# Performance work log

Hardware: AMD Instinct MI355X
Metric: run time of the kernel (lower is better)

## Reference

```python
import jax, jax.numpy as jnp
import numpy as np

B, N, C = 2, 2048, 1024
H = 16
D = C // H  # 64
EPS = 1e-6


def rms_norm(x, w):
    # LlamaRMSNorm: fp32 variance over last dim
    xf = x.astype(jnp.float32)
    var = jnp.mean(xf * xf, axis=-1, keepdims=True)
    xf = xf * jax.lax.rsqrt(var + EPS)
    return (w * xf).astype(x.dtype)


def setup_inputs() -> dict:
    key = jax.random.key(0)
    ks = jax.random.split(key, 4)
    x = jax.random.normal(ks[0], (B, N, C), dtype=jnp.float32)
    mask = jax.random.randint(ks[1], (B, N), 0, 2, dtype=jnp.int32)
    qkv_w = jax.random.normal(ks[2], (3 * C, C), dtype=jnp.float32) * (1.0 / np.sqrt(C))
    qkv_b = jnp.zeros((3 * C,), dtype=jnp.float32)
    proj_w = jax.random.normal(ks[3], (C, C), dtype=jnp.float32) * (1.0 / np.sqrt(C))
    proj_b = jnp.zeros((C,), dtype=jnp.float32)
    qn_w = jnp.ones((D,), dtype=jnp.float32)
    kn_w = jnp.ones((D,), dtype=jnp.float32)
    return {"x": x, "mask": mask, "qkv_w": qkv_w, "qkv_b": qkv_b,
            "proj_w": proj_w, "proj_b": proj_b, "qn_w": qn_w, "kn_w": kn_w}


def reference(x, mask, qkv_w, qkv_b, proj_w, proj_b, qn_w, kn_w):
    dtype = x.dtype
    scale = D ** -0.5
    # qkv projection -> (3, B, H, N, D)
    qkv = (x @ qkv_w.T + qkv_b).reshape(B, N, 3, H, D).transpose(2, 0, 3, 1, 4)
    q, k, v = qkv[0], qkv[1], qkv[2]
    q = rms_norm(q, qn_w)
    k = rms_norm(k, kn_w)
    q = q * scale
    # scores in fp32, key-padding mask [B,1,1,N]
    attn = jnp.einsum('bhnd,bhmd->bhnm', q, k).astype(jnp.float32)
    key_mask = (mask != 0)[:, None, None, :]
    attn = jnp.where(key_mask, attn, jnp.float32(-1e9))
    attn = jax.nn.softmax(attn, axis=-1).astype(dtype)
    out = jnp.einsum('bhnm,bhmd->bhnd', attn, v)  # (B,H,N,D)
    out = out.transpose(0, 2, 1, 3).reshape(B, N, C)
    return out @ proj_w.T + proj_b
```

## Files before the change

### kernel.cpp

```cpp
#include <hip/hip_runtime.h>
#include <hip/hip_bf16.h>
#include <stdint.h>

namespace {

constexpr int kB = 2;
constexpr int kN = 2048;
constexpr int kC = 1024;
constexpr int kH = 16;
constexpr int kD = 64;
constexpr int kTok = kB * kN;
constexpr int k3C  = 3 * kC;
constexpr size_t kPS = (size_t)kTok * k3C;
constexpr size_t kXE = (size_t)kTok * kC;
constexpr size_t kWQ = (size_t)k3C * kC;
constexpr size_t kWP = (size_t)kC * kC;

using bhalf8 = __attribute__((ext_vector_type(8))) __bf16;
using f32x4  = __attribute__((ext_vector_type(4))) float;

__device__ inline unsigned short f2bf(float f) {
  __hip_bfloat16 h = __float2bfloat16(f);
  return *reinterpret_cast<unsigned short*>(&h);
}
__device__ inline float bf2f(unsigned short u) {
  __hip_bfloat16 h;
  *reinterpret_cast<unsigned short*>(&h) = u;
  return __bfloat162float(h);
}
__device__ inline void split2(float v, unsigned short& h, unsigned short& l) {
  const unsigned short hb = f2bf(v);
  h = hb;
  l = f2bf(v - bf2f(hb));
}

__device__ inline void glds16(const unsigned short* g, unsigned short* l) {
  __builtin_amdgcn_global_load_lds(
      (const __attribute__((address_space(1))) void*)g,
      (__attribute__((address_space(3))) void*)l, 16, 0, 0);
}

__global__ __launch_bounds__(256)
void split_planes(const float* __restrict__ src,
                  unsigned short* __restrict__ H,
                  unsigned short* __restrict__ L, int n4)
{
  const int i = blockIdx.x * 256 + threadIdx.x;
  if (i >= n4) return;
  const float4 v = ((const float4*)src)[i];
  ushort4 hh, ll;
  split2(v.x, hh.x, ll.x); split2(v.y, hh.y, ll.y);
  split2(v.z, hh.z, ll.z); split2(v.w, hh.w, ll.w);
  ((ushort4*)H)[i] = hh;
  ((ushort4*)L)[i] = ll;
}

__global__ __launch_bounds__(256)
void vt_transpose(const unsigned short* __restrict__ H,
                  unsigned short* __restrict__ VTH)
{
  const int gw   = blockIdx.x * 4 + (threadIdx.x >> 6);
  const int lane = threadIdx.x & 63;
  const int bh   = gw >> 8;
  const int oct  = gw & 255;
  const int b = bh >> 4, h = bh & 15;
  const int tok0 = oct * 8;
  union { unsigned short u[8]; uint4 v; } ph;
  #pragma unroll
  for (int e = 0; e < 8; ++e) {
    const size_t g = (size_t)(b * kN + tok0 + e) * k3C + 2 * kC + h * kD + lane;
    ph.u[e] = H[g];
  }
  *(uint4*)(&VTH[((size_t)bh * kD + lane) * kN + tok0]) = ph.v;
}

__global__ __launch_bounds__(512)
void gemm_qkv256(const unsigned short* __restrict__ AH,
                 const unsigned short* __restrict__ AL,
                 const unsigned short* __restrict__ WH,
                 const unsigned short* __restrict__ WL,
                 const float* __restrict__ bias,
                 unsigned short* __restrict__ OutH,
                 unsigned short* __restrict__ OutL,
                 const float* __restrict__ qn,
                 const float* __restrict__ kn)
{
  constexpr int BK = 32;
  constexpr int NT = kC / BK;

  __shared__ __align__(16) unsigned short sA[2][2][256 * 32];
  __shared__ __align__(16) unsigned short sB[2][2][256 * 32];

  const int tt   = threadIdx.x;
  const int wave = tt >> 6;
  const int lane = tt & 63;
  const int quad = lane >> 4;
  const int l16  = lane & 15;
  const int bm = blockIdx.x * 256;
  const int bn = blockIdx.y * 256;
  const int wm = (wave >> 2) * 128;
  const int wn = (wave & 3) * 64;

  int srow[2], scol[2];
  #pragma unroll
  for (int r = 0; r < 2; ++r) {
    const int u = r * 512 + tt;
    srow[r] = u >> 2;
    scol[r] = ((u & 3) ^ ((srow[r] >> 1) & 3)) * 8;
  }

  auto stageU = [&](int bf, int k0, int which) {
    const unsigned short* src = (which == 0) ? AH : (which == 1) ? WH
                              : (which == 2) ? WL : AL;
    const int base = (which == 0 || which == 3) ? bm : bn;
    unsigned short* dst = (which == 0) ? &sA[bf][0][0]
                        : (which == 3) ? &sA[bf][1][0]
                        : (which == 1) ? &sB[bf][0][0] : &sB[bf][1][0];
    #pragma unroll
    for (int r = 0; r < 2; ++r)
      glds16(&src[(size_t)(base + srow[r]) * kC + k0 + scol[r]],
             &dst[(r * 512 + tt) * 8]);
  };

  auto rdA = [&](int bf, int pl, int row) -> bhalf8 {
    return *(const bhalf8*)(&sA[bf][pl][row * 32 + ((quad ^ ((row >> 1) & 3)) * 8)]);
  };
  auto rdB = [&](int bf, int pl, int row) -> bhalf8 {
    return *(const bhalf8*)(&sB[bf][pl][row * 32 + ((quad ^ ((row >> 1) & 3)) * 8)]);
  };

  f32x4 acc[8][4] = {};
  bhalf8 ah[8], bh_[4], bl_[4];

  stageU(0, 0, 0); stageU(0, 0, 1); stageU(0, 0, 2); stageU(0, 0, 3);
  asm volatile("s_waitcnt vmcnt(4)" ::: "memory");
  __builtin_amdgcn_sched_barrier(0);
  asm volatile("s_barrier" ::: "memory");

  for (int t = 0; t < NT - 1; ++t) {
    const int buf  = t & 1;
    const int nbuf = buf ^ 1;
    const int nk0  = (t + 1) * BK;

    #pragma unroll
    for (int i = 0; i < 8; ++i) ah[i]  = rdA(buf, 0, wm + i * 16 + l16);
    #pragma unroll
    for (int j = 0; j < 4; ++j) bh_[j] = rdB(buf, 0, wn + j * 16 + l16);
    stageU(nbuf, nk0, 0);
    stageU(nbuf, nk0, 1);
    asm volatile("s_waitcnt vmcnt(6)" ::: "memory");
    __builtin_amdgcn_sched_barrier(0);
    asm volatile("s_barrier" ::: "memory");
    __builtin_amdgcn_s_setprio(1);
    #pragma unroll
    for (int i = 0; i < 8; ++i)
      #pragma unroll
      for (int j = 0; j < 4; ++j)
        acc[i][j] = __builtin_amdgcn_mfma_f32_16x16x32_bf16(ah[i], bh_[j], acc[i][j], 0, 0, 0);
    __builtin_amdgcn_s_setprio(0);

    #pragma unroll
    for (int j = 0; j < 4; ++j) bl_[j] = rdB(buf, 1, wn + j * 16 + l16);
    stageU(nbuf, nk0, 2);
    asm volatile("s_waitcnt vmcnt(6)" ::: "memory");
    __builtin_amdgcn_sched_barrier(0);
    asm volatile("s_barrier" ::: "memory");
    __builtin_amdgcn_s_setprio(1);
    #pragma unroll
    for (int i = 0; i < 8; ++i)
      #pragma unroll
      for (int j = 0; j < 4; ++j)
        acc[i][j] = __builtin_amdgcn_mfma_f32_16x16x32_bf16(ah[i], bl_[j], acc[i][j], 0, 0, 0);
    __builtin_amdgcn_s_setprio(0);

    stageU(nbuf, nk0, 3);
    asm volatile("s_waitcnt vmcnt(4)" ::: "memory");
    __builtin_amdgcn_sched_barrier(0);
    asm volatile("s_barrier" ::: "memory");
    __builtin_amdgcn_s_setprio(1);
    {
      bhalf8 al0[4];
      #pragma unroll
      for (int i = 0; i < 4; ++i) al0[i] = rdA(buf, 1, wm + i * 16 + l16);
      #pragma unroll
      for (int i = 0; i < 4; ++i)
        #pragma unroll
        for (int j = 0; j < 4; ++j)
          acc[i][j] = __builtin_amdgcn_mfma_f32_16x16x32_bf16(al0[i], bh_[j], acc[i][j], 0, 0, 0);
      bhalf8 al1[4];
      #pragma unroll
      for (int i = 0; i < 4; ++i) al1[i] = rdA(buf, 1, wm + (4 + i) * 16 + l16);
      #pragma unroll
      for (int i = 0; i < 4; ++i)
        #pragma unroll
        for (int j = 0; j < 4; ++j)
          acc[4 + i][j] = __builtin_amdgcn_mfma_f32_16x16x32_bf16(al1[i], bh_[j], acc[4 + i][j], 0, 0, 0);
    }
    __builtin_amdgcn_s_setprio(0);
    asm volatile("s_barrier" ::: "memory");
  }

  {
    const int buf = (NT - 1) & 1;
    #pragma unroll
    for (int i = 0; i < 8; ++i) ah[i]  = rdA(buf, 0, wm + i * 16 + l16);
    #pragma unroll
    for (int j = 0; j < 4; ++j) bh_[j] = rdB(buf, 0, wn + j * 16 + l16);
    __builtin_amdgcn_s_setprio(1);
    #pragma unroll
    for (int i = 0; i < 8; ++i)
      #pragma unroll
      for (int j = 0; j < 4; ++j)
        acc[i][j] = __builtin_amdgcn_mfma_f32_16x16x32_bf16(ah[i], bh_[j], acc[i][j], 0, 0, 0);
    __builtin_amdgcn_s_setprio(0);

    asm volatile("s_waitcnt vmcnt(2)" ::: "memory");
    __builtin_amdgcn_sched_barrier(0);
    asm volatile("s_barrier" ::: "memory");
    #pragma unroll
    for (int j = 0; j < 4; ++j) bl_[j] = rdB(buf, 1, wn + j * 16 + l16);
    __builtin_amdgcn_s_setprio(1);
    #pragma unroll
    for (int i = 0; i < 8; ++i)
      #pragma unroll
      for (int j = 0; j < 4; ++j)
        acc[i][j] = __builtin_amdgcn_mfma_f32_16x16x32_bf16(ah[i], bl_[j], acc[i][j], 0, 0, 0);
    __builtin_amdgcn_s_setprio(0);

    asm volatile("s_waitcnt vmcnt(0)" ::: "memory");
    __builtin_amdgcn_sched_barrier(0);
    asm volatile("s_barrier" ::: "memory");
    __builtin_amdgcn_s_setprio(1);
    {
      bhalf8 al0[4];
      #pragma unroll
      for (int i = 0; i < 4; ++i) al0[i] = rdA(buf, 1, wm + i * 16 + l16);
      #pragma unroll
      for (int i = 0; i < 4; ++i)
        #pragma unroll
        for (int j = 0; j < 4; ++j)
          acc[i][j] = __builtin_amdgcn_mfma_f32_16x16x32_bf16(al0[i], bh_[j], acc[i][j], 0, 0, 0);
      bhalf8 al1[4];
      #pragma unroll
      for (int i = 0; i < 4; ++i) al1[i] = rdA(buf, 1, wm + (4 + i) * 16 + l16);
      #pragma unroll
      for (int i = 0; i < 4; ++i)
        #pragma unroll
        for (int j = 0; j < 4; ++j)
          acc[4 + i][j] = __builtin_amdgcn_mfma_f32_16x16x32_bf16(al1[i], bh_[j], acc[4 + i][j], 0, 0, 0);
    }
    __builtin_amdgcn_s_setprio(0);
  }

  const int slice = bn >> 10;
  const bool writeL = (slice == 0);
  float bv[4], wv[4];
  #pragma unroll
  for (int j = 0; j < 4; ++j) {
    bv[j] = bias[bn + wn + j * 16 + l16];
    if (slice < 2) wv[j] = (slice ? kn : qn)[j * 16 + l16];
  }

  #pragma unroll
  for (int i = 0; i < 8; ++i) {
    float val[4][4];
    #pragma unroll
    for (int j = 0; j < 4; ++j)
      #pragma unroll
      for (int r = 0; r < 4; ++r)
        val[j][r] = acc[i][j][r] + bv[j];

    if (slice < 2) {
      #pragma unroll
      for (int r = 0; r < 4; ++r) {
        float ss = val[0][r] * val[0][r];
        #pragma unroll
        for (int j = 1; j < 4; ++j) ss += val[j][r] * val[j][r];
        #pragma unroll
        for (int d = 1; d < 16; d <<= 1) ss += __shfl_xor(ss, d, 64);
        float rinv = rsqrtf(ss * (1.0f / 64.0f) + 1e-6f);
        if (slice == 0) rinv *= 0.125f;
        #pragma unroll
        for (int j = 0; j < 4; ++j) val[j][r] = wv[j] * (val[j][r] * rinv);
      }
    }

    #pragma unroll
    for (int j = 0; j < 4; ++j) {
      const int n = bn + wn + j * 16 + l16;
      #pragma unroll
      for (int r = 0; r < 4; ++r) {
        const int m = bm + wm + i * 16 + quad * 4 + r;
        unsigned short hh, ll;
        split2(val[j][r], hh, ll);
        OutH[(size_t)m * k3C + n] = hh;
        if (writeL) OutL[(size_t)m * k3C + n] = ll;
      }
    }
  }
}

template<bool OUTF32, bool FUSE_NORM>
__global__ __launch_bounds__(256)
void gemm_planes(const unsigned short* __restrict__ AH,
                 const unsigned short* __restrict__ AL, int lda,
                 const unsigned short* __restrict__ WH,
                 const unsigned short* __restrict__ WL,
                 const float* __restrict__ bias,
                 float* __restrict__ OutF,
                 unsigned short* __restrict__ OutH,
                 unsigned short* __restrict__ OutL,
                 const float* __restrict__ qn,
                 const float* __restrict__ kn,
                 int Nn, int K)
{
  __shared__ __align__(16) unsigned short AsH[128 * 32], AsL[128 * 32];
  __shared__ __align__(16) unsigned short BsH[128 * 32], BsL[128 * 32];

  const int t    = threadIdx.x;
  const int wave = t >> 6;
  const int lane = t & 63;
  const int quad = lane >> 4;
  const int l16  = lane & 15;
  const int bm = blockIdx.x * 128;
  const int bn = blockIdx.y * 128;
  const int wm = (wave >> 1) * 64;
  const int wn = (wave & 1) * 64;

  f32x4 acc[4][4] = {};

  for (int k0 = 0; k0 < K; k0 += 32) {
    #pragma unroll
    for (int r = 0; r < 2; ++r) {
      const int c   = r * 256 + t;
      const int row = c >> 2;
      const int col = (c & 3) * 8;
      glds16(&AH[(size_t)(bm + row) * lda + k0 + col], &AsH[c * 8]);
      glds16(&AL[(size_t)(bm + row) * lda + k0 + col], &AsL[c * 8]);
      glds16(&WH[(size_t)(bn + row) * K + k0 + col], &BsH[c * 8]);
      glds16(&WL[(size_t)(bn + row) * K + k0 + col], &BsL[c * 8]);
    }
    __syncthreads();

    bhalf8 afh[4], afl[4], bgh[4], bgl[4];
    #pragma unroll
    for (int i = 0; i < 4; ++i) {
      afh[i] = *(const bhalf8*)(&AsH[(wm + i * 16 + l16) * 32 + quad * 8]);
      afl[i] = *(const bhalf8*)(&AsL[(wm + i * 16 + l16) * 32 + quad * 8]);
      bgh[i] = *(const bhalf8*)(&BsH[(wn + i * 16 + l16) * 32 + quad * 8]);
      bgl[i] = *(const bhalf8*)(&BsL[(wn + i * 16 + l16) * 32 + quad * 8]);
    }
    #pragma unroll
    for (int i = 0; i < 4; ++i)
      #pragma unroll
      for (int j = 0; j < 4; ++j) {
        f32x4 a = acc[i][j];
        a = __builtin_amdgcn_mfma_f32_16x16x32_bf16(afh[i], bgh[j], a, 0, 0, 0);
        a = __builtin_amdgcn_mfma_f32_16x16x32_bf16(afh[i], bgl[j], a, 0, 0, 0);
        a = __builtin_amdgcn_mfma_f32_16x16x32_bf16(afl[i], bgh[j], a, 0, 0, 0);
        acc[i][j] = a;
      }
    __syncthreads();
  }

  float bv[4], wv[4];
  const int slice = FUSE_NORM ? (bn >> 10) : 0;
  const bool writeL = !FUSE_NORM || slice == 0;
  #pragma unroll
  for (int j = 0; j < 4; ++j) {
    bv[j] = bias[bn + wn + j * 16 + l16];
    if (FUSE_NORM && slice < 2)
      wv[j] = (slice ? kn : qn)[j * 16 + l16];
  }

  #pragma unroll
  for (int i = 0; i < 4; ++i) {
    float val[4][4];
    #pragma unroll
    for (int j = 0; j < 4; ++j)
      #pragma unroll
      for (int r = 0; r < 4; ++r)
        val[j][r] = acc[i][j][r] + bv[j];

    if (FUSE_NORM && slice < 2) {
      #pragma unroll
      for (int r = 0; r < 4; ++r) {
        float ss = val[0][r] * val[0][r];
        #pragma unroll
        for (int j = 1; j < 4; ++j) ss += val[j][r] * val[j][r];
        #pragma unroll
        for (int d = 1; d < 16; d <<= 1) ss += __shfl_xor(ss, d, 64);
        float rinv = rsqrtf(ss * (1.0f / 64.0f) + 1e-6f);
        if (slice == 0) rinv *= 0.125f;
        #pragma unroll
        for (int j = 0; j < 4; ++j) val[j][r] = wv[j] * (val[j][r] * rinv);
      }
    }

    #pragma unroll
    for (int j = 0; j < 4; ++j) {
      const int n = bn + wn + j * 16 + l16;
      #pragma unroll
      for (int r = 0; r < 4; ++r) {
        const int m = bm + wm + i * 16 + quad * 4 + r;
        if (OUTF32) {
          OutF[(size_t)m * Nn + n] = val[j][r];
        } else {
          unsigned short hh, ll;
          split2(val[j][r], hh, ll);
          OutH[(size_t)m * Nn + n] = hh;
          if (writeL) OutL[(size_t)m * Nn + n] = ll;
        }
      }
    }
  }
}

__global__ __launch_bounds__(256)
void attn_kernel(unsigned short* __restrict__ H, unsigned short* __restrict__ L,
                 const unsigned short* __restrict__ VTH,
                 const int* __restrict__ mask)
{
  constexpr int P = 72;
  __shared__ __align__(16) unsigned short KtH[64 * P];
  __shared__ __align__(16) unsigned short VtH[64 * P];
  __shared__ __align__(16) unsigned short Pt[4][32 * P];

  const int t    = threadIdx.x;
  const int wave = t >> 6;
  const int lane = t & 63;
  const int quad = lane >> 4;
  const int l16  = lane & 15;

  const int lin  = blockIdx.x;
  const int xcd  = lin & 7;
  const int slot = lin >> 3;
  const int bh   = xcd + 8 * (slot >> 4);
  const int qblk = slot & 15;
  const int b  = bh >> 4;
  const int h  = bh & 15;
  const int q0 = qblk * 128 + wave * 32;

  const int row0 = t >> 3,         col0 = (t & 7) * 8;
  const int row1 = (256 + t) >> 3, col1 = ((256 + t) & 7) * 8;

  bhalf8 qfh[2][2], qfl[2][2];
  #pragma unroll
  for (int g = 0; g < 2; ++g) {
    const size_t qrow = (size_t)(b * kN + q0 + g * 16 + l16) * k3C + h * kD;
    qfh[g][0] = *(const bhalf8*)(&H[qrow + quad * 8]);
    qfh[g][1] = *(const bhalf8*)(&H[qrow + 32 + quad * 8]);
    qfl[g][0] = *(const bhalf8*)(&L[qrow + quad * 8]);
    qfl[g][1] = *(const bhalf8*)(&L[qrow + 32 + quad * 8]);
  }

  f32x4 acc_o[2][4] = {};
  float lpart[2][4] = {};

  uint4 sk0, sk1, sv0, sv1;
  int mcur[4], mnext[4];

  auto pref = [&](int kt) {
    sk0 = *(const uint4*)(&H[(size_t)(b * kN + kt + row0) * k3C + kC + h * kD + col0]);
    sk1 = *(const uint4*)(&H[(size_t)(b * kN + kt + row1) * k3C + kC + h * kD + col1]);
    sv0 = *(const uint4*)(&VTH[((size_t)bh * kD + row0) * kN + kt + col0]);
    sv1 = *(const uint4*)(&VTH[((size_t)bh * kD + row1) * kN + kt + col1]);
  };
  auto loadM = [&](int kt, int* m) {
    #pragma unroll
    for (int nt = 0; nt < 4; ++nt) m[nt] = mask[b * kN + kt + nt * 16 + l16];
  };

  pref(0);
  loadM(0, mcur);

  for (int i = 0; i < 32; ++i) {
    const int kt = i * 64;
    *(uint4*)(&KtH[row0 * P + col0]) = sk0;
    *(uint4*)(&KtH[row1 * P + col1]) = sk1;
    *(uint4*)(&VtH[row0 * P + col0]) = sv0;
    *(uint4*)(&VtH[row1 * P + col1]) = sv1;
    __syncthreads();

    if (i < 31) { pref(kt + 64); loadM(kt + 64, mnext); }

    #pragma unroll
    for (int nt = 0; nt < 4; ++nt) {
      const int kr = (nt * 16 + l16) * P + quad * 8;
      const bhalf8 kh0 = *(const bhalf8*)(&KtH[kr]);
      const bhalf8 kh1 = *(const bhalf8*)(&KtH[kr + 32]);
      const float flag = mcur[nt] ? 1.0f : 0.0f;
      #pragma unroll
      for (int g = 0; g < 2; ++g) {
        f32x4 s = {};
        s = __builtin_amdgcn_mfma_f32_16x16x32_bf16(qfh[g][0], kh0, s, 0, 0, 0);
        s = __builtin_amdgcn_mfma_f32_16x16x32_bf16(qfh[g][1], kh1, s, 0, 0, 0);
        s = __builtin_amdgcn_mfma_f32_16x16x32_bf16(qfl[g][0], kh0, s, 0, 0, 0);
        s = __builtin_amdgcn_mfma_f32_16x16x32_bf16(qfl[g][1], kh1, s, 0, 0, 0);
        #pragma unroll
        for (int r = 0; r < 4; ++r) {
          const float p = flag * __expf(s[r]);
          lpart[g][r] += p;
          Pt[wave][(g * 16 + quad * 4 + r) * P + nt * 16 + l16] = f2bf(p);
        }
      }
    }

    #pragma unroll
    for (int kk = 0; kk < 2; ++kk) {
      const bhalf8 pa0 = *(const bhalf8*)(&Pt[wave][l16 * P + kk * 32 + quad * 8]);
      const bhalf8 pa1 = *(const bhalf8*)(&Pt[wave][(16 + l16) * P + kk * 32 + quad * 8]);
      #pragma unroll
      for (int dt = 0; dt < 4; ++dt) {
        const bhalf8 vb = *(const bhalf8*)(&VtH[(dt * 16 + l16) * P + kk * 32 + quad * 8]);
        acc_o[0][dt] = __builtin_amdgcn_mfma_f32_16x16x32_bf16(pa0, vb, acc_o[0][dt], 0, 0, 0);
        acc_o[1][dt] = __builtin_amdgcn_mfma_f32_16x16x32_bf16(pa1, vb, acc_o[1][dt], 0, 0, 0);
      }
    }

    #pragma unroll
    for (int nt = 0; nt < 4; ++nt) mcur[nt] = mnext[nt];
    __syncthreads();
  }

  #pragma unroll
  for (int g = 0; g < 2; ++g)
    #pragma unroll
    for (int r = 0; r < 4; ++r) {
      float s = lpart[g][r];
      #pragma unroll
      for (int d = 1; d < 16; d <<= 1) s += __shfl_xor(s, d, 64);
      lpart[g][r] = s;
    }
  #pragma unroll
  for (int g = 0; g < 2; ++g)
    #pragma unroll
    for (int dt = 0; dt < 4; ++dt)
      #pragma unroll
      for (int r = 0; r < 4; ++r) {
        const int qrow = q0 + g * 16 + quad * 4 + r;
        const float inv = 1.0f / fmaxf(lpart[g][r], 1.0e-30f);
        const size_t off = (size_t)(b * kN + qrow) * k3C + h * kD + dt * 16 + l16;
        unsigned short hh, ll;
        split2(acc_o[g][dt][r] * inv, hh, ll);
        H[off] = hh; L[off] = ll;
      }
}

}

extern "C" void kernel_launch(void* const* d_in, const int* in_sizes, int n_in,
                              void* d_out, int out_size, void* d_ws, size_t ws_size,
                              hipStream_t stream)
{
  const float* x      = (const float*)d_in[0];
  const int*   maskp  = (const int*)d_in[1];
  const float* qkv_w  = (const float*)d_in[2];
  const float* qkv_b  = (const float*)d_in[3];
  const float* proj_w = (const float*)d_in[4];
  const float* proj_b = (const float*)d_in[5];
  const float* qn_w   = (const float*)d_in[6];
  const float* kn_w   = (const float*)d_in[7];
  float* out = (float*)d_out;

  unsigned short* qH = (unsigned short*)d_ws;
  unsigned short* qL = qH + kPS;
  unsigned short* R1 = qL + kPS;
  unsigned short* R2 = R1 + 2 * kXE;
  unsigned short* xH = R1,  *xL = R1 + kXE;
  unsigned short* VTH = R1;
  unsigned short* wqH = R2, *wqL = R2 + kWQ;
  unsigned short* wpH = R2, *wpL = R2 + kWP;

  split_planes<<<(int)(kXE / 4 / 256), 256, 0, stream>>>(x, xH, xL, (int)(kXE / 4));
  split_planes<<<(int)(kWQ / 4 / 256), 256, 0, stream>>>(qkv_w, wqH, wqL, (int)(kWQ / 4));

  gemm_qkv256<<<dim3(kTok / 256, k3C / 256), 512, 0, stream>>>(
      xH, xL, wqH, wqL, qkv_b, qH, qL, qn_w, kn_w);

  vt_transpose<<<2048, 256, 0, stream>>>(qH, VTH);
  split_planes<<<(int)(kWP / 4 / 256), 256, 0, stream>>>(proj_w, wpH, wpL, (int)(kWP / 4));

  attn_kernel<<<dim3(512), 256, 0, stream>>>(qH, qL, VTH, maskp);

  gemm_planes<true, false><<<dim3(kTok / 128, kC / 128), 256, 0, stream>>>(
      qH, qL, k3C, wpH, wpL, proj_b, out, nullptr, nullptr, nullptr, nullptr, kC, kC);
}
```

Baseline: 299.7 us.

## Halve attention query tile per block, swizzle K/V LDS, fold log2e into Q scale

The attention kernel now gives each wave 16 query rows instead of 32 and launches 1024 blocks instead of 512, which raises parallelism and cuts per-wave register use. The price is that every K/V tile is loaded from global memory twice as often. The K and V shared-memory tiles use an XOR swizzle on columns to reduce LDS bank conflicts. The Q scale now includes log2(e), so exp2f can replace __expf, which is valid because there is no max subtraction.

```diff
diff --git a/kernel.cpp b/kernel.cpp
--- a/kernel.cpp
+++ b/kernel.cpp
@@ -1,6 +1,7 @@
 #include <hip/hip_runtime.h>
 #include <hip/hip_bf16.h>
 #include <stdint.h>
+#include <math.h>
 
 namespace {
 
@@ -279,7 +280,7 @@
         #pragma unroll
         for (int d = 1; d < 16; d <<= 1) ss += __shfl_xor(ss, d, 64);
         float rinv = rsqrtf(ss * (1.0f / 64.0f) + 1e-6f);
-        if (slice == 0) rinv *= 0.125f;
+        if (slice == 0) rinv *= 0.18033688011112042f;
         #pragma unroll
         for (int j = 0; j < 4; ++j) val[j][r] = wv[j] * (val[j][r] * rinv);
       }
@@ -424,7 +425,7 @@
   constexpr int P = 72;
   __shared__ __align__(16) unsigned short KtH[64 * P];
   __shared__ __align__(16) unsigned short VtH[64 * P];
-  __shared__ __align__(16) unsigned short Pt[4][32 * P];
+  __shared__ __align__(16) unsigned short Pt[4][16 * P];
 
   const int t    = threadIdx.x;
   const int wave = t >> 6;
@@ -435,36 +436,37 @@
   const int lin  = blockIdx.x;
   const int xcd  = lin & 7;
   const int slot = lin >> 3;
-  const int bh   = xcd + 8 * (slot >> 4);
-  const int qblk = slot & 15;
+  const int bh   = xcd + 8 * (slot >> 5);
+  const int qblk = slot & 31;
   const int b  = bh >> 4;
   const int h  = bh & 15;
-  const int q0 = qblk * 128 + wave * 32;
-
-  const int row0 = t >> 3,         col0 = (t & 7) * 8;
-  const int row1 = (256 + t) >> 3, col1 = ((256 + t) & 7) * 8;
-
-  bhalf8 qfh[2][2], qfl[2][2];
-  #pragma unroll
-  for (int g = 0; g < 2; ++g) {
-    const size_t qrow = (size_t)(b * kN + q0 + g * 16 + l16) * k3C + h * kD;
-    qfh[g][0] = *(const bhalf8*)(&H[qrow + quad * 8]);
-    qfh[g][1] = *(const bhalf8*)(&H[qrow + 32 + quad * 8]);
-    qfl[g][0] = *(const bhalf8*)(&L[qrow + quad * 8]);
-    qfl[g][1] = *(const bhalf8*)(&L[qrow + 32 + quad * 8]);
-  }
-
-  f32x4 acc_o[2][4] = {};
-  float lpart[2][4] = {};
+  const int q0 = qblk * 64 + wave * 16;
+
+  const int row0 = t >> 3, col0 = (t & 7) * 8;
+  const int row1 = row0 + 32;
+  const int sw0  = (row0 & 7) << 3;
+  const int sc0  = col0 ^ sw0;
+
+  bhalf8 qfh[2], qfl[2];
+  {
+    const size_t qrow = (size_t)(b * kN + q0 + l16) * k3C + h * kD;
+    qfh[0] = *(const bhalf8*)(&H[qrow + quad * 8]);
+    qfh[1] = *(const bhalf8*)(&H[qrow + 32 + quad * 8]);
+    qfl[0] = *(const bhalf8*)(&L[qrow + quad * 8]);
+    qfl[1] = *(const bhalf8*)(&L[qrow + 32 + quad * 8]);
+  }
+
+  f32x4 acc_o[4] = {};
+  float lpart[4] = {};
 
   uint4 sk0, sk1, sv0, sv1;
   int mcur[4], mnext[4];
 
   auto pref = [&](int kt) {
     sk0 = *(const uint4*)(&H[(size_t)(b * kN + kt + row0) * k3C + kC + h * kD + col0]);
-    sk1 = *(const uint4*)(&H[(size_t)(b * kN + kt + row1) * k3C + kC + h * kD + col1]);
+    sk1 = *(const uint4*)(&H[(size_t)(b * kN + kt + row1) * k3C + kC + h * kD + col0]);
     sv0 = *(const uint4*)(&VTH[((size_t)bh * kD + row0) * kN + kt + col0]);
-    sv1 = *(const uint4*)(&VTH[((size_t)bh * kD + row1) * kN + kt + col1]);
+    sv1 = *(const uint4*)(&VTH[((size_t)bh * kD + row1) * kN + kt + col0]);
   };
   auto loadM = [&](int kt, int* m) {
     #pragma unroll
@@ -473,48 +475,46 @@
 
   pref(0);
   loadM(0, mcur);
+  #pragma unroll
+  for (int nt = 0; nt < 4; ++nt) mnext[nt] = mcur[nt];
 
   for (int i = 0; i < 32; ++i) {
     const int kt = i * 64;
-    *(uint4*)(&KtH[row0 * P + col0]) = sk0;
-    *(uint4*)(&KtH[row1 * P + col1]) = sk1;
-    *(uint4*)(&VtH[row0 * P + col0]) = sv0;
-    *(uint4*)(&VtH[row1 * P + col1]) = sv1;
+    *(uint4*)(&KtH[row0 * P + sc0]) = sk0;
+    *(uint4*)(&KtH[row1 * P + sc0]) = sk1;
+    *(uint4*)(&VtH[row0 * P + sc0]) = sv0;
+    *(uint4*)(&VtH[row1 * P + sc0]) = sv1;
     __syncthreads();
 
     if (i < 31) { pref(kt + 64); loadM(kt + 64, mnext); }
 
+    const int rsw = (l16 & 7) << 3;
     #pragma unroll
     for (int nt = 0; nt < 4; ++nt) {
-      const int kr = (nt * 16 + l16) * P + quad * 8;
-      const bhalf8 kh0 = *(const bhalf8*)(&KtH[kr]);
-      const bhalf8 kh1 = *(const bhalf8*)(&KtH[kr + 32]);
+      const int kr = (nt * 16 + l16) * P;
+      const bhalf8 kh0 = *(const bhalf8*)(&KtH[kr + ((quad * 8) ^ rsw)]);
+      const bhalf8 kh1 = *(const bhalf8*)(&KtH[kr + ((32 + quad * 8) ^ rsw)]);
       const float flag = mcur[nt] ? 1.0f : 0.0f;
-      #pragma unroll
-      for (int g = 0; g < 2; ++g) {
-        f32x4 s = {};
-        s = __builtin_amdgcn_mfma_f32_16x16x32_bf16(qfh[g][0], kh0, s, 0, 0, 0);
-        s = __builtin_amdgcn_mfma_f32_16x16x32_bf16(qfh[g][1], kh1, s, 0, 0, 0);
-        s = __builtin_amdgcn_mfma_f32_16x16x32_bf16(qfl[g][0], kh0, s, 0, 0, 0);
-        s = __builtin_amdgcn_mfma_f32_16x16x32_bf16(qfl[g][1], kh1, s, 0, 0, 0);
-        #pragma unroll
-        for (int r = 0; r < 4; ++r) {
-          const float p = flag * __expf(s[r]);
-          lpart[g][r] += p;
-          Pt[wave][(g * 16 + quad * 4 + r) * P + nt * 16 + l16] = f2bf(p);
-        }
+      f32x4 s = {};
+      s = __builtin_amdgcn_mfma_f32_16x16x32_bf16(qfh[0], kh0, s, 0, 0, 0);
+      s = __builtin_amdgcn_mfma_f32_16x16x32_bf16(qfh[1], kh1, s, 0, 0, 0);
+      s = __builtin_amdgcn_mfma_f32_16x16x32_bf16(qfl[0], kh0, s, 0, 0, 0);
+      s = __builtin_amdgcn_mfma_f32_16x16x32_bf16(qfl[1], kh1, s, 0, 0, 0);
+      #pragma unroll
+      for (int r = 0; r < 4; ++r) {
+        const float p = flag * exp2f(s[r]);
+        lpart[r] += p;
+        Pt[wave][(quad * 4 + r) * P + nt * 16 + l16] = f2bf(p);
       }
     }
 
     #pragma unroll
     for (int kk = 0; kk < 2; ++kk) {
-      const bhalf8 pa0 = *(const bhalf8*)(&Pt[wave][l16 * P + kk * 32 + quad * 8]);
-      const bhalf8 pa1 = *(const bhalf8*)(&Pt[wave][(16 + l16) * P + kk * 32 + quad * 8]);
+      const bhalf8 pa = *(const bhalf8*)(&Pt[wave][l16 * P + kk * 32 + quad * 8]);
       #pragma unroll
       for (int dt = 0; dt < 4; ++dt) {
-        const bhalf8 vb = *(const bhalf8*)(&VtH[(dt * 16 + l16) * P + kk * 32 + quad * 8]);
-        acc_o[0][dt] = __builtin_amdgcn_mfma_f32_16x16x32_bf16(pa0, vb, acc_o[0][dt], 0, 0, 0);
-        acc_o[1][dt] = __builtin_amdgcn_mfma_f32_16x16x32_bf16(pa1, vb, acc_o[1][dt], 0, 0, 0);
+        const bhalf8 vb = *(const bhalf8*)(&VtH[(dt * 16 + l16) * P + ((kk * 32 + quad * 8) ^ rsw)]);
+        acc_o[dt] = __builtin_amdgcn_mfma_f32_16x16x32_bf16(pa, vb, acc_o[dt], 0, 0, 0);
       }
     }
 
@@ -524,27 +524,23 @@
   }
 
   #pragma unroll
-  for (int g = 0; g < 2; ++g)
+  for (int r = 0; r < 4; ++r) {
+    float s = lpart[r];
+    #pragma unroll
+    for (int d = 1; d < 16; d <<= 1) s += __shfl_xor(s, d, 64);
+    lpart[r] = s;
+  }
+  #pragma unroll
+  for (int dt = 0; dt < 4; ++dt)
     #pragma unroll
     for (int r = 0; r < 4; ++r) {
-      float s = lpart[g][r];
-      #pragma unroll
-      for (int d = 1; d < 16; d <<= 1) s += __shfl_xor(s, d, 64);
-      lpart[g][r] = s;
-    }
-  #pragma unroll
-  for (int g = 0; g < 2; ++g)
-    #pragma unroll
-    for (int dt = 0; dt < 4; ++dt)
-      #pragma unroll
-      for (int r = 0; r < 4; ++r) {
-        const int qrow = q0 + g * 16 + quad * 4 + r;
-        const float inv = 1.0f / fmaxf(lpart[g][r], 1.0e-30f);
-        const size_t off = (size_t)(b * kN + qrow) * k3C + h * kD + dt * 16 + l16;
-        unsigned short hh, ll;
-        split2(acc_o[g][dt][r] * inv, hh, ll);
-        H[off] = hh; L[off] = ll;
-      }
+      const int qrow = q0 + quad * 4 + r;
+      const float inv = 1.0f / fmaxf(lpart[r], 1.0e-30f);
+      const size_t off = (size_t)(b * kN + qrow) * k3C + h * kD + dt * 16 + l16;
+      unsigned short hh, ll;
+      split2(acc_o[dt][r] * inv, hh, ll);
+      H[off] = hh; L[off] = ll;
+    }
 }
 
 }
@@ -581,7 +577,7 @@
   vt_transpose<<<2048, 256, 0, stream>>>(qH, VTH);
   split_planes<<<(int)(kWP / 4 / 256), 256, 0, stream>>>(proj_w, wpH, wpL, (int)(kWP / 4));
 
-  attn_kernel<<<dim3(512), 256, 0, stream>>>(qH, qL, VTH, maskp);
+  attn_kernel<<<dim3(1024), 256, 0, stream>>>(qH, qL, VTH, maskp);
 
   gemm_planes<true, false><<<dim3(kTok / 128, kC / 128), 256, 0, stream>>>(
       qH, qL, k3C, wpH, wpL, proj_b, out, nullptr, nullptr, nullptr, nullptr, kC, kC);
```

After: 320.2 us. +6.9%, slower.

## Double-buffer K/V shared tiles, fold log2e into q scale, pad P tile

Applied to the files above, without the earlier changes.

Double-buffers the K and V tiles in LDS. The next tile is stored into the alternate buffer after the current tile's compute, and the global prefetch runs two tiles ahead, so each iteration needs one barrier instead of two. The q scale now includes log2(e), so the softmax can use exp2f instead of __expf, and the P scratch row pitch changes from 72 to 68 to alter the LDS bank mapping. The cost is more LDS use, which may lower occupancy, and some extra live registers for the prefetched data.

```diff
diff --git a/kernel.cpp b/kernel.cpp
--- a/kernel.cpp
+++ b/kernel.cpp
@@ -1,6 +1,7 @@
 #include <hip/hip_runtime.h>
 #include <hip/hip_bf16.h>
 #include <stdint.h>
+#include <math.h>
 
 namespace {
 
@@ -279,7 +280,7 @@
         #pragma unroll
         for (int d = 1; d < 16; d <<= 1) ss += __shfl_xor(ss, d, 64);
         float rinv = rsqrtf(ss * (1.0f / 64.0f) + 1e-6f);
-        if (slice == 0) rinv *= 0.125f;
+        if (slice == 0) rinv *= 0.18033688011112042f;
         #pragma unroll
         for (int j = 0; j < 4; ++j) val[j][r] = wv[j] * (val[j][r] * rinv);
       }
@@ -421,10 +422,11 @@
                  const unsigned short* __restrict__ VTH,
                  const int* __restrict__ mask)
 {
-  constexpr int P = 72;
-  __shared__ __align__(16) unsigned short KtH[64 * P];
-  __shared__ __align__(16) unsigned short VtH[64 * P];
-  __shared__ __align__(16) unsigned short Pt[4][32 * P];
+  constexpr int P   = 72;
+  constexpr int Ppt = 68;
+  __shared__ __align__(16) unsigned short KtH[2][64 * P];
+  __shared__ __align__(16) unsigned short VtH[2][64 * P];
+  __shared__ __align__(16) unsigned short Pt[4][32 * Ppt];
 
   const int t    = threadIdx.x;
   const int wave = t >> 6;
@@ -466,6 +468,12 @@
     sv0 = *(const uint4*)(&VTH[((size_t)bh * kD + row0) * kN + kt + col0]);
     sv1 = *(const uint4*)(&VTH[((size_t)bh * kD + row1) * kN + kt + col1]);
   };
+  auto store_tile = [&](int bf) {
+    *(uint4*)(&KtH[bf][row0 * P + col0]) = sk0;
+    *(uint4*)(&KtH[bf][row1 * P + col1]) = sk1;
+    *(uint4*)(&VtH[bf][row0 * P + col0]) = sv0;
+    *(uint4*)(&VtH[bf][row1 * P + col1]) = sv1;
+  };
   auto loadM = [&](int kt, int* m) {
     #pragma unroll
     for (int nt = 0; nt < 4; ++nt) m[nt] = mask[b * kN + kt + nt * 16 + l16];
@@ -473,22 +481,22 @@
 
   pref(0);
   loadM(0, mcur);
+  #pragma unroll
+  for (int nt = 0; nt < 4; ++nt) mnext[nt] = mcur[nt];
+  store_tile(0);
+  pref(64);
+  __syncthreads();
 
   for (int i = 0; i < 32; ++i) {
+    const int cur = i & 1;
     const int kt = i * 64;
-    *(uint4*)(&KtH[row0 * P + col0]) = sk0;
-    *(uint4*)(&KtH[row1 * P + col1]) = sk1;
-    *(uint4*)(&VtH[row0 * P + col0]) = sv0;
-    *(uint4*)(&VtH[row1 * P + col1]) = sv1;
-    __syncthreads();
-
-    if (i < 31) { pref(kt + 64); loadM(kt + 64, mnext); }
+    if (i < 31) loadM(kt + 64, mnext);
 
     #pragma unroll
     for (int nt = 0; nt < 4; ++nt) {
       const int kr = (nt * 16 + l16) * P + quad * 8;
-      const bhalf8 kh0 = *(const bhalf8*)(&KtH[kr]);
-      const bhalf8 kh1 = *(const bhalf8*)(&KtH[kr + 32]);
+      const bhalf8 kh0 = *(const bhalf8*)(&KtH[cur][kr]);
+      const bhalf8 kh1 = *(const bhalf8*)(&KtH[cur][kr + 32]);
       const float flag = mcur[nt] ? 1.0f : 0.0f;
       #pragma unroll
       for (int g = 0; g < 2; ++g) {
@@ -499,28 +507,32 @@
         s = __builtin_amdgcn_mfma_f32_16x16x32_bf16(qfl[g][1], kh1, s, 0, 0, 0);
         #pragma unroll
         for (int r = 0; r < 4; ++r) {
-          const float p = flag * __expf(s[r]);
+          const float p = flag * exp2f(s[r]);
           lpart[g][r] += p;
-          Pt[wave][(g * 16 + quad * 4 + r) * P + nt * 16 + l16] = f2bf(p);
+          Pt[wave][(g * 16 + quad * 4 + r) * Ppt + nt * 16 + l16] = f2bf(p);
         }
       }
     }
 
     #pragma unroll
     for (int kk = 0; kk < 2; ++kk) {
-      const bhalf8 pa0 = *(const bhalf8*)(&Pt[wave][l16 * P + kk * 32 + quad * 8]);
-      const bhalf8 pa1 = *(const bhalf8*)(&Pt[wave][(16 + l16) * P + kk * 32 + quad * 8]);
+      const bhalf8 pa0 = *(const bhalf8*)(&Pt[wave][l16 * Ppt + kk * 32 + quad * 8]);
+      const bhalf8 pa1 = *(const bhalf8*)(&Pt[wave][(16 + l16) * Ppt + kk * 32 + quad * 8]);
       #pragma unroll
       for (int dt = 0; dt < 4; ++dt) {
-        const bhalf8 vb = *(const bhalf8*)(&VtH[(dt * 16 + l16) * P + kk * 32 + quad * 8]);
+        const bhalf8 vb = *(const bhalf8*)(&VtH[cur][(dt * 16 + l16) * P + kk * 32 + quad * 8]);
         acc_o[0][dt] = __builtin_amdgcn_mfma_f32_16x16x32_bf16(pa0, vb, acc_o[0][dt], 0, 0, 0);
         acc_o[1][dt] = __builtin_amdgcn_mfma_f32_16x16x32_bf16(pa1, vb, acc_o[1][dt], 0, 0, 0);
       }
     }
 
-    #pragma unroll
-    for (int nt = 0; nt < 4; ++nt) mcur[nt] = mnext[nt];
-    __syncthreads();
+    if (i < 31) {
+      store_tile(cur ^ 1);
+      if (i < 30) pref(kt + 128);
+      __syncthreads();
+      #pragma unroll
+      for (int nt = 0; nt < 4; ++nt) mcur[nt] = mnext[nt];
+    }
   }
 
   #pragma unroll
```

After: 306.0 us. 1.02x slower.
